# Kernel optimization log

Hardware: AMD Instinct MI355X
Metric: run time of the kernel (lower is better)

The kernel has to match this reference:

```python
import jax, jax.numpy as jnp
import numpy as np

N = 50000      # nodes
E = 800000     # edges (before self loops)
F_IN = 50      # PPI num_features
H = 4          # heads
C = 64         # hidden per head
NC = 121       # PPI num_classes
NEG_SLOPE = 0.2


def setup_inputs() -> dict:
    key = jax.random.key(0)
    ks = jax.random.split(key, 20)
    p = lambda k, shape: (jax.random.normal(k, shape, jnp.float32) * 0.1)
    x0 = jax.random.normal(ks[0], (N, F_IN), jnp.float32)
    edge_index = jax.random.randint(ks[1], (2, E), 0, N, dtype=jnp.int64)
    return dict(
        x0=x0, edge_index=edge_index,
        W1=p(ks[2], (F_IN, H * C)), as1=p(ks[3], (H, C)), ad1=p(ks[4], (H, C)),
        res1=p(ks[5], (F_IN, H * C)), b1=jnp.zeros((H * C,), jnp.float32),
        W2=p(ks[6], (H * C, H * C)), as2=p(ks[7], (H, C)), ad2=p(ks[8], (H, C)),
        res2=p(ks[9], (H * C, H * C)), b2=jnp.zeros((H * C,), jnp.float32),
        W3=p(ks[10], (H * C, H * NC)), as3=p(ks[11], (H, NC)), ad3=p(ks[12], (H, NC)),
        res3=p(ks[13], (H * C, NC)), b3=jnp.zeros((NC,), jnp.float32),
    )


def _gat(x, src, dst, W, a_src, a_dst, resW, b, concat):
    """PyG-style GATConv with residual, self loops already in (src, dst)."""
    n = x.shape[0]
    heads, outc = a_src.shape
    h = (x @ W).reshape(n, heads, outc)                 # [N,H,C]
    al_s = (h * a_src).sum(-1)                          # [N,H]
    al_d = (h * a_dst).sum(-1)                          # [N,H]
    e = jax.nn.leaky_relu(al_s[src] + al_d[dst], NEG_SLOPE)  # [E,H]
    m = jax.ops.segment_max(e, dst, num_segments=n)     # stable softmax per dst
    ex = jnp.exp(e - m[dst])
    denom = jax.ops.segment_sum(ex, dst, num_segments=n)
    alpha = ex / denom[dst]                             # [E,H]
    out = jax.ops.segment_sum(h[src] * alpha[:, :, None], dst, num_segments=n)  # [N,H,C]
    out = out.reshape(n, heads * outc) if concat else out.mean(axis=1)
    return out + x @ resW + b


def reference(x0, edge_index,
              W1, as1, ad1, res1, b1,
              W2, as2, ad2, res2, b2,
              W3, as3, ad3, res3, b3):
    n = x0.shape[0]
    loop = jnp.arange(n, dtype=edge_index.dtype)        # add self loops (PyG default)
    src = jnp.concatenate([edge_index[0], loop])
    dst = jnp.concatenate([edge_index[1], loop])
    x1 = jax.nn.relu(_gat(x0, src, dst, W1, as1, ad1, res1, b1, True))
    x2 = jax.nn.relu(_gat(x1, src, dst, W2, as2, ad2, res2, b2, True))
    x3 = _gat(x2, src, dst, W3, as3, ad3, res3, b3, False)
    return x3
```

## Files before the change

kernel.cpp:

```cpp
#include <hip/hip_runtime.h>

#define NNODES 50000
#define NEDGES 800000
#define NTOT   (NEDGES + NNODES)
#define F_IN   50
#define KPAD1  64
#define HEADS  4
#define C1     64
#define HC1    256
#define NC     121
#define K1S    320
#define K3S    1280
#define N2S    512
#define N2X    520
#define SLOTS  128

typedef unsigned short ushort_t;
typedef __attribute__((ext_vector_type(4))) unsigned short ushort4_t;
typedef __attribute__((ext_vector_type(8))) unsigned short ushort8;
typedef __attribute__((ext_vector_type(8))) __bf16 bf16x8;
typedef __attribute__((ext_vector_type(4))) float f32x4;
typedef __attribute__((ext_vector_type(4))) int int4_t;

__device__ __forceinline__ ushort_t f2bf(float f) {
    union { float f; unsigned int u; } v; v.f = f;
    unsigned int u = v.u;
    return (ushort_t)((u + 0x7fffu + ((u >> 16) & 1u)) >> 16);
}
__device__ __forceinline__ float bf2f(ushort_t s) {
    union { unsigned int u; float f; } v; v.u = ((unsigned int)s) << 16;
    return v.f;
}
__device__ __forceinline__ float lrelu(float x) { return x > 0.f ? x : 0.2f * x; }
__device__ __forceinline__ f32x4 cvt4lo(ushort8 v) {
    f32x4 r; r[0] = bf2f(v[0]); r[1] = bf2f(v[1]); r[2] = bf2f(v[2]); r[3] = bf2f(v[3]);
    return r;
}
__device__ __forceinline__ f32x4 cvt4hi(ushort8 v) {
    f32x4 r; r[0] = bf2f(v[4]); r[1] = bf2f(v[5]); r[2] = bf2f(v[6]); r[3] = bf2f(v[7]);
    return r;
}
__device__ __forceinline__ void wave_lds_sync() {
    asm volatile("s_waitcnt lgkmcnt(0)" ::: "memory");
}

__device__ __forceinline__ void scatter_body(int i, const int* __restrict__ ei,
                                             int* __restrict__ cnt,
                                             int* __restrict__ csr_src) {
    if (i >= NTOT) return;
    int s, d;
    if (i < NEDGES) { s = ei[i]; d = ei[NEDGES + i]; }
    else            { s = d = i - NEDGES; }
    if ((unsigned)d >= NNODES) d = 0;
    if ((unsigned)s >= NNODES) s = 0;
    int k = atomicAdd(&cnt[d], 1);
    if (k < SLOTS) csr_src[d * SLOTS + k] = s;
}

#define SZ_A (NNODES * KPAD1)
#define SZ_B (HC1 * K1S)
#define SZ_C (N2X * HC1)
#define SZ_D (N2X)
#define SZ_E (NC * K3S)
#define SZ_F (KPAD1 * 4)
#define SZ_G (HC1 * 4)
#define PREP_TOTAL (SZ_A + SZ_B + SZ_C + SZ_D + SZ_E + 2 * SZ_F + 2 * SZ_G)
#define PREP_BLK ((PREP_TOTAL + 255) / 256)
#define CNT_BLK  ((NTOT + 255) / 256)

__device__ void prep_body(int i,
                 const float* __restrict__ x0,
                 const float* __restrict__ W1, const float* __restrict__ res1,
                 const float* __restrict__ W2, const float* __restrict__ res2,
                 const float* __restrict__ W3, const float* __restrict__ res3,
                 const float* __restrict__ as1, const float* __restrict__ ad1,
                 const float* __restrict__ as2, const float* __restrict__ ad2,
                 const float* __restrict__ as3, const float* __restrict__ ad3,
                 const float* __restrict__ b2,
                 ushort_t* __restrict__ x0b, ushort_t* __restrict__ Bt1,
                 ushort_t* __restrict__ Bt2, ushort_t* __restrict__ Bt3,
                 float* __restrict__ bias520,
                 float* __restrict__ w_as1, float* __restrict__ w_ad1,
                 float* __restrict__ w_as3, float* __restrict__ w_ad3) {
    if (i < SZ_A) {
        int m = i >> 6, k = i & 63;
        x0b[i] = (k < F_IN) ? f2bf(x0[(size_t)m * F_IN + k]) : (ushort_t)0;
        return;
    }
    i -= SZ_A;
    if (i < SZ_B) {
        int c = i / K1S, kk = i - c * K1S;
        float v = 0.f;
        if (kk < 256) {
            int h = kk >> 6, k = kk & 63;
            if (k < F_IN && (c >> 6) == h) v = W1[(size_t)k * HC1 + c];
        } else {
            int k = kk - 256;
            if (k < F_IN) v = res1[(size_t)k * HC1 + c];
        }
        Bt1[i] = f2bf(v);
        return;
    }
    i -= SZ_B;
    if (i < SZ_C) {
        int c = i / HC1, k = i - c * HC1;
        float v;
        if (c < HC1) {
            v = W2[(size_t)k * HC1 + c];
        } else if (c < 512) {
            v = res2[(size_t)k * HC1 + (c - HC1)];
        } else {
            int j = c - 512;
            int h = j & 3;
            const float* a = (j < 4) ? as2 : ad2;
            float s = 0.f;
            for (int cc = 0; cc < C1; ++cc)
                s += W2[(size_t)k * HC1 + h * C1 + cc] * a[h * C1 + cc];
            v = s;
        }
        Bt2[i] = f2bf(v);
        return;
    }
    i -= SZ_C;
    if (i < SZ_D) {
        bias520[i] = (i >= HC1 && i < 512) ? b2[i - HC1] : 0.f;
        return;
    }
    i -= SZ_D;
    if (i < SZ_E) {
        int c = i / K3S, kk = i - c * K3S;
        float v;
        if (kk < 1024) {
            int h = kk >> 8, k = kk & 255;
            v = 0.25f * W3[(size_t)k * (HEADS * NC) + h * NC + c];
        } else {
            int k = kk - 1024;
            v = res3[(size_t)k * NC + c];
        }
        Bt3[i] = f2bf(v);
        return;
    }
    i -= SZ_E;
    if (i < 2 * SZ_F) {
        const float* a = (i < SZ_F) ? as1 : ad1;
        float* w = (i < SZ_F) ? w_as1 : w_ad1;
        int ii = (i < SZ_F) ? i : i - SZ_F;
        int k = ii >> 2, h = ii & 3;
        float s = 0.f;
        if (k < F_IN)
            for (int c = 0; c < C1; ++c) s += W1[(size_t)k * HC1 + h * C1 + c] * a[h * C1 + c];
        w[ii] = s;
        return;
    }
    i -= 2 * SZ_F;
    {
        int grp = i / SZ_G, ii = i - grp * SZ_G;
        int k = ii >> 2, h = ii & 3;
        const float* a = grp ? ad3 : as3;
        float s = 0.f;
        for (int c = 0; c < NC; ++c)
            s += W3[(size_t)k * (HEADS * NC) + h * NC + c] * a[h * NC + c];
        (grp ? w_ad3 : w_as3)[ii] = s;
    }
}

__global__ __launch_bounds__(256)
void prep_scatter_kernel(const float* __restrict__ x0,
                 const float* __restrict__ W1, const float* __restrict__ res1,
                 const float* __restrict__ W2, const float* __restrict__ res2,
                 const float* __restrict__ W3, const float* __restrict__ res3,
                 const float* __restrict__ as1, const float* __restrict__ ad1,
                 const float* __restrict__ as2, const float* __restrict__ ad2,
                 const float* __restrict__ as3, const float* __restrict__ ad3,
                 const float* __restrict__ b2,
                 ushort_t* __restrict__ x0b, ushort_t* __restrict__ Bt1,
                 ushort_t* __restrict__ Bt2, ushort_t* __restrict__ Bt3,
                 float* __restrict__ bias520,
                 float* __restrict__ w_as1, float* __restrict__ w_ad1,
                 float* __restrict__ w_as3, float* __restrict__ w_ad3,
                 const int* __restrict__ ei, int* __restrict__ cnt,
                 int* __restrict__ csr_src) {
    int b = blockIdx.x;
    if (b < PREP_BLK) {
        prep_body(b * 256 + threadIdx.x, x0, W1, res1, W2, res2, W3, res3,
                  as1, ad1, as2, ad2, as3, ad3, b2, x0b, Bt1, Bt2, Bt3,
                  bias520, w_as1, w_ad1, w_as3, w_ad3);
    } else {
        scatter_body((b - PREP_BLK) * 256 + threadIdx.x, ei, cnt, csr_src);
    }
}

#define BK 64
#define LDP (BK + 8)

__global__ __launch_bounds__(256)
void gemm64_kernel(const ushort_t* __restrict__ A1, int lda1,
                   const ushort_t* __restrict__ A2, int lda2, int Ksplit,
                   const ushort_t* __restrict__ Bt, const float* __restrict__ bias,
                   ushort_t* __restrict__ Cb,
                   int M, int N, int K, int relu) {
    __shared__ ushort_t As[64 * LDP];
    __shared__ ushort_t Bs[128 * LDP];
    int tid = threadIdx.x, lane = tid & 63, wid = tid >> 6;
    int l15 = lane & 15, q8 = (lane >> 4) * 8;
    int m0 = blockIdx.y * 64, n0 = blockIdx.x * 128;
    f32x4 c4[8] = {};
    for (int k0 = 0; k0 < K; k0 += BK) {
        #pragma unroll
        for (int it = 0; it < 2; ++it) {
            int c = tid + it * 256;
            int row = c >> 3, c8 = c & 7;
            int k = k0 + c8 * 8;
            ushort8 va = (ushort8)0;
            int gm = m0 + row;
            if (gm < M) {
                if (k < Ksplit) va = *(const ushort8*)&A1[(size_t)gm * lda1 + k];
                else            va = *(const ushort8*)&A2[(size_t)gm * lda2 + (k - Ksplit)];
            }
            *(ushort8*)&As[row * LDP + c8 * 8] = va;
        }
        #pragma unroll
        for (int it = 0; it < 4; ++it) {
            int c = tid + it * 256;
            int row = c >> 3, c8 = c & 7;
            int k = k0 + c8 * 8;
            ushort8 vb = (ushort8)0;
            int gn = n0 + row;
            if (gn < N) vb = *(const ushort8*)&Bt[(size_t)gn * K + k];
            *(ushort8*)&Bs[row * LDP + c8 * 8] = vb;
        }
        __syncthreads();
        #pragma unroll
        for (int kk = 0; kk < BK; kk += 32) {
            bf16x8 af = *(const bf16x8*)&As[(wid * 16 + l15) * LDP + kk + q8];
            #pragma unroll
            for (int ni = 0; ni < 8; ++ni) {
                bf16x8 bf = *(const bf16x8*)&Bs[(ni * 16 + l15) * LDP + kk + q8];
                c4[ni] = __builtin_amdgcn_mfma_f32_16x16x32_bf16(af, bf, c4[ni], 0, 0, 0);
            }
        }
        __syncthreads();
    }
    int rbase = m0 + wid * 16 + (lane >> 4) * 4;
    #pragma unroll
    for (int ni = 0; ni < 8; ++ni) {
        int col = n0 + ni * 16 + l15;
        if (col >= N) continue;
        float bv = bias ? bias[col] : 0.f;
        #pragma unroll
        for (int r = 0; r < 4; ++r) {
            int m = rbase + r;
            if (m >= M) continue;
            float v = c4[ni][r] + bv;
            if (relu) v = fmaxf(v, 0.f);
            Cb[(size_t)m * N + col] = f2bf(v);
        }
    }
}

__global__ __launch_bounds__(256)
void gemm2x64_kernel(const ushort_t* __restrict__ A,
                     const ushort_t* __restrict__ Bt,
                     const float* __restrict__ bias,
                     ushort_t* __restrict__ comb,
                     float* __restrict__ als, float* __restrict__ ald,
                     int M) {
    __shared__ ushort_t As[64 * LDP];
    __shared__ ushort_t Bs[128 * LDP];
    int tid = threadIdx.x, lane = tid & 63, wid = tid >> 6;
    int l15 = lane & 15, q8 = (lane >> 4) * 8;
    int m0 = blockIdx.y * 64, n0 = blockIdx.x * 128;
    f32x4 c4[8] = {};
    for (int k0 = 0; k0 < HC1; k0 += BK) {
        #pragma unroll
        for (int it = 0; it < 2; ++it) {
            int c = tid + it * 256;
            int row = c >> 3, c8 = c & 7;
            int k = k0 + c8 * 8;
            ushort8 va = (ushort8)0;
            int gm = m0 + row;
            if (gm < M) va = *(const ushort8*)&A[(size_t)gm * HC1 + k];
            *(ushort8*)&As[row * LDP + c8 * 8] = va;
        }
        #pragma unroll
        for (int it = 0; it < 4; ++it) {
            int c = tid + it * 256;
            int row = c >> 3, c8 = c & 7;
            int k = k0 + c8 * 8;
            ushort8 vb = (ushort8)0;
            int gn = n0 + row;
            if (gn < N2X) vb = *(const ushort8*)&Bt[(size_t)gn * HC1 + k];
            *(ushort8*)&Bs[row * LDP + c8 * 8] = vb;
        }
        __syncthreads();
        #pragma unroll
        for (int kk = 0; kk < BK; kk += 32) {
            bf16x8 af = *(const bf16x8*)&As[(wid * 16 + l15) * LDP + kk + q8];
            #pragma unroll
            for (int ni = 0; ni < 8; ++ni) {
                bf16x8 bf = *(const bf16x8*)&Bs[(ni * 16 + l15) * LDP + kk + q8];
                c4[ni] = __builtin_amdgcn_mfma_f32_16x16x32_bf16(af, bf, c4[ni], 0, 0, 0);
            }
        }
        __syncthreads();
    }
    int rbase = m0 + wid * 16 + (lane >> 4) * 4;
    #pragma unroll
    for (int ni = 0; ni < 8; ++ni) {
        int ncol = n0 + ni * 16 + l15;
        if (ncol >= N2X) continue;
        float bv = bias[ncol];
        #pragma unroll
        for (int r = 0; r < 4; ++r) {
            int m = rbase + r;
            if (m >= M) continue;
            float v = c4[ni][r] + bv;
            if (ncol < 512) {
                comb[(size_t)m * N2S + ncol] = f2bf(v);
            } else {
                int j = ncol - 512;
                if (j < 4) als[m * 4 + j] = v;
                else       ald[m * 4 + (j - 4)] = v;
            }
        }
    }
}

__global__ __launch_bounds__(256)
void gemm3s_kernel(const ushort_t* __restrict__ A1, int lda1,
                   const ushort_t* __restrict__ A2, int lda2, int Ksplit,
                   const ushort_t* __restrict__ Bt, const float* __restrict__ bias,
                   float* __restrict__ out, int M, int N, int K) {
    __shared__ ushort_t As[64 * LDP];
    __shared__ ushort_t Bs[128 * LDP];
    int tid = threadIdx.x, lane = tid & 63, wid = tid >> 6;
    int l15 = lane & 15, q8 = (lane >> 4) * 8;
    int m0 = blockIdx.x * 64;
    f32x4 c4[8] = {};
    for (int k0 = 0; k0 < K; k0 += BK) {
        #pragma unroll
        for (int it = 0; it < 2; ++it) {
            int c = tid + it * 256;
            int row = c >> 3, c8 = c & 7;
            int k = k0 + c8 * 8;
            ushort8 va = (ushort8)0;
            int gm = m0 + row;
            if (gm < M) {
                if (k < Ksplit) va = *(const ushort8*)&A1[(size_t)gm * lda1 + k];
                else            va = *(const ushort8*)&A2[(size_t)gm * lda2 + (k - Ksplit)];
            }
            *(ushort8*)&As[row * LDP + c8 * 8] = va;
        }
        #pragma unroll
        for (int it = 0; it < 4; ++it) {
            int c = tid + it * 256;
            int row = c >> 3, c8 = c & 7;
            int k = k0 + c8 * 8;
            ushort8 vb = (ushort8)0;
            if (row < N) vb = *(const ushort8*)&Bt[(size_t)row * K + k];
            *(ushort8*)&Bs[row * LDP + c8 * 8] = vb;
        }
        __syncthreads();
        #pragma unroll
        for (int kk = 0; kk < BK; kk += 32) {
            bf16x8 af = *(const bf16x8*)&As[(wid * 16 + l15) * LDP + kk + q8];
            #pragma unroll
            for (int ni = 0; ni < 8; ++ni) {
                bf16x8 bf = *(const bf16x8*)&Bs[(ni * 16 + l15) * LDP + kk + q8];
                c4[ni] = __builtin_amdgcn_mfma_f32_16x16x32_bf16(af, bf, c4[ni], 0, 0, 0);
            }
        }
        __syncthreads();
    }
    int rbase = m0 + wid * 16 + (lane >> 4) * 4;
    #pragma unroll
    for (int ni = 0; ni < 8; ++ni) {
        int col = ni * 16 + l15;
        if (col >= NC) continue;
        float bv = bias[col];
        #pragma unroll
        for (int r = 0; r < 4; ++r) {
            int m = rbase + r;
            if (m < M) out[(size_t)m * NC + col] = c4[ni][r] + bv;
        }
    }
}

__global__ __launch_bounds__(256)
void logits_gemv_kernel(const ushort_t* __restrict__ X, int K,
                        const float* __restrict__ w_as, const float* __restrict__ w_ad,
                        float* __restrict__ als, float* __restrict__ ald) {
    int wid = threadIdx.x >> 6, lane = threadIdx.x & 63;
    int n = blockIdx.x * 4 + wid;
    float ps[HEADS] = {}, pd[HEADS] = {};
    for (int k0 = lane * 4; k0 < K; k0 += 256) {
        ushort4_t xv = *(const ushort4_t*)&X[(size_t)n * K + k0];
        float x[4] = {bf2f(xv.x), bf2f(xv.y), bf2f(xv.z), bf2f(xv.w)};
        #pragma unroll
        for (int j = 0; j < 4; ++j) {
            #pragma unroll
            for (int h = 0; h < HEADS; ++h) {
                ps[h] += x[j] * w_as[(k0 + j) * 4 + h];
                pd[h] += x[j] * w_ad[(k0 + j) * 4 + h];
            }
        }
    }
    #pragma unroll
    for (int off = 32; off; off >>= 1)
        #pragma unroll
        for (int h = 0; h < HEADS; ++h) {
            ps[h] += __shfl_xor(ps[h], off);
            pd[h] += __shfl_xor(pd[h], off);
        }
    if (lane == 0)
        #pragma unroll
        for (int h = 0; h < HEADS; ++h) {
            als[n * HEADS + h] = ps[h];
            ald[n * HEADS + h] = pd[h];
        }
}

#define E_CHUNK32(ROWBYTES)                                                   \
    int i = base + l;                                                         \
    int nv = end - base; if (nv > 32) nv = 32;                                \
    if (i < end) {                                                            \
        int s = csr_src[i];                                                   \
        soffw[l] = s * (ROWBYTES);                                            \
        f32x4 av = *(const f32x4*)&als[s * 4];                                \
        f32x4 e;                                                              \
        _Pragma("unroll")                                                     \
        for (int h = 0; h < HEADS; ++h) {                                     \
            e[h] = __expf(lrelu(av[h] + aldd[h]));                            \
            den4[h] += e[h];                                                  \
        }                                                                     \
        *(f32x4*)&sew[l * 4] = e;                                             \
    }                                                                         \
    wave_lds_sync();

#define DEN_REDUCE16                                                          \
    _Pragma("unroll")                                                         \
    for (int off = 16; off; off >>= 1)                                        \
        _Pragma("unroll")                                                     \
        for (int h = 0; h < HEADS; ++h)                                       \
            den4[h] += __shfl_xor(den4[h], off);

__global__ __launch_bounds__(256)
void agg1_kernel(const ushort_t* __restrict__ x0b,
                 const float* __restrict__ als, const float* __restrict__ ald,
                 const int* __restrict__ cnt, const int* __restrict__ csr_src,
                 ushort_t* __restrict__ aggx) {
    __shared__ int   soff[8][32];
    __shared__ float se[8][32 * 4];
    int tid = threadIdx.x;
    int hw = tid >> 5, l = tid & 31;
    int d = blockIdx.x * 8 + hw;
    int* soffw = soff[hw];
    float* sew = se[hw];
    int beg = d * SLOTS;
    int deg = cnt[d]; if (deg > SLOTS) deg = SLOTS;
    int end = beg + deg;
    f32x4 aldd = *(const f32x4*)&ald[d * 4];
    f32x4 den4 = (f32x4)0.f;
    f32x4 acc0 = (f32x4)0.f, acc1 = (f32x4)0.f;
    int lb = l * 4;
    for (int base = beg; base < end; base += 32) {
        E_CHUNK32(KPAD1 * 2)
        int j = 0;
        for (; j + 4 <= nv; j += 4) {
            int4_t o = *(const int4_t*)&soffw[j];
            f32x4 e0 = *(const f32x4*)&sew[j * 4];
            f32x4 e1 = *(const f32x4*)&sew[(j + 1) * 4];
            f32x4 e2 = *(const f32x4*)&sew[(j + 2) * 4];
            f32x4 e3 = *(const f32x4*)&sew[(j + 3) * 4];
            unsigned int v0 = *(const unsigned int*)((const char*)x0b + o.x + lb);
            unsigned int v1 = *(const unsigned int*)((const char*)x0b + o.y + lb);
            unsigned int v2 = *(const unsigned int*)((const char*)x0b + o.z + lb);
            unsigned int v3 = *(const unsigned int*)((const char*)x0b + o.w + lb);
            acc0 += e0 * bf2f((ushort_t)(v0 & 0xffffu)) + e1 * bf2f((ushort_t)(v1 & 0xffffu))
                  + e2 * bf2f((ushort_t)(v2 & 0xffffu)) + e3 * bf2f((ushort_t)(v3 & 0xffffu));
            acc1 += e0 * bf2f((ushort_t)(v0 >> 16)) + e1 * bf2f((ushort_t)(v1 >> 16))
                  + e2 * bf2f((ushort_t)(v2 >> 16)) + e3 * bf2f((ushort_t)(v3 >> 16));
        }
        for (; j < nv; ++j) {
            int o = soffw[j];
            f32x4 e = *(const f32x4*)&sew[j * 4];
            unsigned int v = *(const unsigned int*)((const char*)x0b + o + lb);
            acc0 += e * bf2f((ushort_t)(v & 0xffffu));
            acc1 += e * bf2f((ushort_t)(v >> 16));
        }
        wave_lds_sync();
    }
    DEN_REDUCE16
    #pragma unroll
    for (int h = 0; h < HEADS; ++h) {
        float r = 1.f / den4[h];
        unsigned int pk = (unsigned int)f2bf(acc0[h] * r)
                        | ((unsigned int)f2bf(acc1[h] * r) << 16);
        *(unsigned int*)&aggx[(size_t)d * HC1 + h * 64 + l * 2] = pk;
    }
}

__global__ __launch_bounds__(256)
void agg2_kernel(const ushort_t* __restrict__ comb,
                 const float* __restrict__ als, const float* __restrict__ ald,
                 const int* __restrict__ cnt, const int* __restrict__ csr_src,
                 const float* __restrict__ w_as3, const float* __restrict__ w_ad3,
                 ushort_t* __restrict__ xnext,
                 float* __restrict__ als3, float* __restrict__ ald3) {
    __shared__ int   soff[8][32];
    __shared__ float se[8][32 * 4];
    int tid = threadIdx.x;
    int hw = tid >> 5, l = tid & 31;
    int d = blockIdx.x * 8 + hw;
    int* soffw = soff[hw];
    float* sew = se[hw];
    int hh = l >> 3;
    int beg = d * SLOTS;
    int deg = cnt[d]; if (deg > SLOTS) deg = SLOTS;
    int end = beg + deg;
    f32x4 aldd = *(const f32x4*)&ald[d * 4];
    f32x4 den4 = (f32x4)0.f;
    f32x4 acc[2] = {};
    int lb = l * 16;
    for (int base = beg; base < end; base += 32) {
        E_CHUNK32(N2S * 2)
        int j = 0;
        for (; j + 4 <= nv; j += 4) {
            int4_t o = *(const int4_t*)&soffw[j];
            ushort8 v0 = *(const ushort8*)((const char*)comb + o.x + lb);
            ushort8 v1 = *(const ushort8*)((const char*)comb + o.y + lb);
            ushort8 v2 = *(const ushort8*)((const char*)comb + o.z + lb);
            ushort8 v3 = *(const ushort8*)((const char*)comb + o.w + lb);
            float e0 = sew[j * 4 + hh], e1 = sew[(j + 1) * 4 + hh];
            float e2 = sew[(j + 2) * 4 + hh], e3 = sew[(j + 3) * 4 + hh];
            acc[0] += e0 * cvt4lo(v0) + e1 * cvt4lo(v1) + e2 * cvt4lo(v2) + e3 * cvt4lo(v3);
            acc[1] += e0 * cvt4hi(v0) + e1 * cvt4hi(v1) + e2 * cvt4hi(v2) + e3 * cvt4hi(v3);
        }
        for (; j < nv; ++j) {
            int o = soffw[j];
            float e = sew[j * 4 + hh];
            ushort8 v = *(const ushort8*)((const char*)comb + o + lb);
            acc[0] += e * cvt4lo(v);
            acc[1] += e * cvt4hi(v);
        }
        wave_lds_sync();
    }
    DEN_REDUCE16
    float r = 1.f / den4[hh];
    ushort8 rv = *(const ushort8*)&comb[(size_t)d * N2S + 256 + l * 8];
    float vout[8];
    ushort8 o8;
    #pragma unroll
    for (int q = 0; q < 2; ++q)
        #pragma unroll
        for (int c = 0; c < 4; ++c) {
            float vv = fmaxf(acc[q][c] * r + bf2f(rv[q * 4 + c]), 0.f);
            vout[q * 4 + c] = vv;
            o8[q * 4 + c] = f2bf(vv);
        }
    *(ushort8*)&xnext[(size_t)d * HC1 + l * 8] = o8;
    f32x4 ps = (f32x4)0.f, pd = (f32x4)0.f;
    #pragma unroll
    for (int cc = 0; cc < 8; ++cc) {
        int col = l * 8 + cc;
        f32x4 wsj = *(const f32x4*)&w_as3[col * 4];
        f32x4 wdj = *(const f32x4*)&w_ad3[col * 4];
        ps += vout[cc] * wsj;
        pd += vout[cc] * wdj;
    }
    #pragma unroll
    for (int off = 16; off; off >>= 1) {
        #pragma unroll
        for (int h = 0; h < HEADS; ++h) {
            ps[h] += __shfl_xor(ps[h], off);
            pd[h] += __shfl_xor(pd[h], off);
        }
    }
    if (l == 0) {
        *(f32x4*)&als3[d * 4] = ps;
        *(f32x4*)&ald3[d * 4] = pd;
    }
}

__global__ __launch_bounds__(256)
void agg3_kernel(const ushort_t* __restrict__ x2b,
                 const float* __restrict__ als, const float* __restrict__ ald,
                 const int* __restrict__ cnt, const int* __restrict__ csr_src,
                 ushort_t* __restrict__ aggx) {
    __shared__ int   soff[8][32];
    __shared__ float se[8][32 * 4];
    int tid = threadIdx.x;
    int hw = tid >> 5, l = tid & 31;
    int d = blockIdx.x * 8 + hw;
    int* soffw = soff[hw];
    float* sew = se[hw];
    int beg = d * SLOTS;
    int deg = cnt[d]; if (deg > SLOTS) deg = SLOTS;
    int end = beg + deg;
    f32x4 aldd = *(const f32x4*)&ald[d * 4];
    f32x4 den4 = (f32x4)0.f;
    f32x4 acc[HEADS][2] = {};
    int lb = l * 16;
    for (int base = beg; base < end; base += 32) {
        E_CHUNK32(HC1 * 2)
        int j = 0;
        for (; j + 4 <= nv; j += 4) {
            int4_t o = *(const int4_t*)&soffw[j];
            ushort8 v0 = *(const ushort8*)((const char*)x2b + o.x + lb);
            ushort8 v1 = *(const ushort8*)((const char*)x2b + o.y + lb);
            ushort8 v2 = *(const ushort8*)((const char*)x2b + o.z + lb);
            ushort8 v3 = *(const ushort8*)((const char*)x2b + o.w + lb);
            f32x4 e0 = *(const f32x4*)&sew[j * 4];
            f32x4 e1 = *(const f32x4*)&sew[(j + 1) * 4];
            f32x4 e2 = *(const f32x4*)&sew[(j + 2) * 4];
            f32x4 e3 = *(const f32x4*)&sew[(j + 3) * 4];
            f32x4 xl, xh;
            xl = cvt4lo(v0); xh = cvt4hi(v0);
            #pragma unroll
            for (int h = 0; h < HEADS; ++h) { acc[h][0] += e0[h] * xl; acc[h][1] += e0[h] * xh; }
            xl = cvt4lo(v1); xh = cvt4hi(v1);
            #pragma unroll
            for (int h = 0; h < HEADS; ++h) { acc[h][0] += e1[h] * xl; acc[h][1] += e1[h] * xh; }
            xl = cvt4lo(v2); xh = cvt4hi(v2);
            #pragma unroll
            for (int h = 0; h < HEADS; ++h) { acc[h][0] += e2[h] * xl; acc[h][1] += e2[h] * xh; }
            xl = cvt4lo(v3); xh = cvt4hi(v3);
            #pragma unroll
            for (int h = 0; h < HEADS; ++h) { acc[h][0] += e3[h] * xl; acc[h][1] += e3[h] * xh; }
        }
        for (; j < nv; ++j) {
            int o = soffw[j];
            f32x4 e = *(const f32x4*)&sew[j * 4];
            ushort8 v = *(const ushort8*)((const char*)x2b + o + lb);
            f32x4 xl = cvt4lo(v), xh = cvt4hi(v);
            #pragma unroll
            for (int h = 0; h < HEADS; ++h) { acc[h][0] += e[h] * xl; acc[h][1] += e[h] * xh; }
        }
        wave_lds_sync();
    }
    DEN_REDUCE16
    #pragma unroll
    for (int h = 0; h < HEADS; ++h) {
        float rdv = 1.f / den4[h];
        ushort8 ow;
        #pragma unroll
        for (int q = 0; q < 2; ++q)
            #pragma unroll
            for (int c = 0; c < 4; ++c)
                ow[q * 4 + c] = f2bf(acc[h][q][c] * rdv);
        *(ushort8*)&aggx[(size_t)d * 1024 + h * HC1 + l * 8] = ow;
    }
}

extern "C" void kernel_launch(void* const* d_in, const int* in_sizes, int n_in,
                              void* d_out, int out_size, void* d_ws, size_t ws_size,
                              hipStream_t stream) {
    const float* x0   = (const float*)d_in[0];
    const int*   ei   = (const int*)d_in[1];
    const float* W1   = (const float*)d_in[2];
    const float* as1  = (const float*)d_in[3];
    const float* ad1  = (const float*)d_in[4];
    const float* res1 = (const float*)d_in[5];
    const float* b1   = (const float*)d_in[6];
    const float* W2   = (const float*)d_in[7];
    const float* as2  = (const float*)d_in[8];
    const float* ad2  = (const float*)d_in[9];
    const float* res2 = (const float*)d_in[10];
    const float* b2   = (const float*)d_in[11];
    const float* W3   = (const float*)d_in[12];
    const float* as3  = (const float*)d_in[13];
    const float* ad3  = (const float*)d_in[14];
    const float* res3 = (const float*)d_in[15];
    const float* b3   = (const float*)d_in[16];

    char* p = (char*)d_ws;
    auto alloc = [&](size_t bytes) -> void* {
        void* r = (void*)p;
        p += (bytes + 255) & ~(size_t)255;
        return r;
    };
    int*      cnt     = (int*)alloc((size_t)NNODES * 4);
    int*      csr_src = (int*)alloc((size_t)NNODES * SLOTS * 4);
    float*    als     = (float*)alloc((size_t)NNODES * HEADS * 4);
    float*    ald     = (float*)alloc((size_t)NNODES * HEADS * 4);
    float*    als3    = (float*)alloc((size_t)NNODES * HEADS * 4);
    float*    ald3    = (float*)alloc((size_t)NNODES * HEADS * 4);
    ushort_t* x0b     = (ushort_t*)alloc((size_t)NNODES * KPAD1 * 2);
    ushort_t* x2      = (ushort_t*)alloc((size_t)NNODES * HC1 * 2);
    ushort_t* Bt1     = (ushort_t*)alloc((size_t)HC1 * K1S * 2);
    ushort_t* Bt2     = (ushort_t*)alloc((size_t)N2X * HC1 * 2);
    float*    bias520 = (float*)alloc((size_t)N2X * 4);
    ushort_t* Bt3     = (ushort_t*)alloc((size_t)NC * K3S * 2);
    float*    w_as1   = (float*)alloc((size_t)KPAD1 * 4 * 4);
    float*    w_ad1   = (float*)alloc((size_t)KPAD1 * 4 * 4);
    float*    w_as3   = (float*)alloc((size_t)HC1 * 4 * 4);
    float*    w_ad3   = (float*)alloc((size_t)HC1 * 4 * 4);
    char*     big     = (char*)alloc((size_t)NNODES * 1024 * 2);
    ushort_t* aggx1   = (ushort_t*)big;
    ushort_t* x1      = (ushort_t*)(big + (size_t)NNODES * HC1 * 2);
    ushort_t* comb    = (ushort_t*)(big + (size_t)NNODES * HC1 * 4);
    ushort_t* aggx3   = (ushort_t*)big;

    hipMemsetAsync(cnt, 0, (size_t)NNODES * 4, stream);

    prep_scatter_kernel<<<PREP_BLK + CNT_BLK, 256, 0, stream>>>(
        x0, W1, res1, W2, res2, W3, res3, as1, ad1, as2, ad2, as3, ad3, b2,
        x0b, Bt1, Bt2, Bt3, bias520, w_as1, w_ad1, w_as3, w_ad3,
        ei, cnt, csr_src);

    int nagg4 = NNODES / 4;
    int nagg8 = NNODES / 8;
    int mblk  = (NNODES + 63) / 64;

    logits_gemv_kernel<<<nagg4, 256, 0, stream>>>(x0b, KPAD1, w_as1, w_ad1, als, ald);
    agg1_kernel<<<nagg8, 256, 0, stream>>>(x0b, als, ald, cnt, csr_src, aggx1);
    {
        dim3 g(HC1 / 128, mblk);
        gemm64_kernel<<<g, 256, 0, stream>>>(aggx1, HC1, x0b, KPAD1, HC1,
                                             Bt1, b1, x1, NNODES, HC1, K1S, 1);
    }

    {
        dim3 g((N2X + 127) / 128, mblk);
        gemm2x64_kernel<<<g, 256, 0, stream>>>(x1, Bt2, bias520, comb, als, ald, NNODES);
    }
    agg2_kernel<<<nagg8, 256, 0, stream>>>(comb, als, ald, cnt, csr_src,
                                           w_as3, w_ad3, x2, als3, ald3);

    agg3_kernel<<<nagg8, 256, 0, stream>>>(x2, als3, ald3, cnt, csr_src, aggx3);
    gemm3s_kernel<<<mblk, 256, 0, stream>>>(
        aggx3, 1024, x2, HC1, 1024, Bt3, b3, (float*)d_out, NNODES, 128, K3S);
}
```

Baseline: 537.3 us.

## Fuse layer-1 attention logits into prep kernel and pad edge counters

Removes the separate layer-1 logits GEMV launch. The attention-folded weights are now computed per block in LDS and the logits are produced directly from fp32 x0 inside the combined prep/scatter kernel. The per-node degree counters are padded to 16-int stride to reduce atomic contention and false sharing, and scatter blocks are ordered first in the grid. In exchange, every gemv block recomputes the 400 small weight dot products, the cnt buffer and its memset grow 16x, and later kernels read counters strided.

```diff
diff --git a/kernel.cpp b/kernel.cpp
--- a/kernel.cpp
+++ b/kernel.cpp
@@ -14,6 +14,7 @@
 #define N2S    512
 #define N2X    520
 #define SLOTS  128
+#define CPAD   16
 
 typedef unsigned short ushort_t;
 typedef __attribute__((ext_vector_type(4))) unsigned short ushort4_t;
@@ -53,7 +54,7 @@
     else            { s = d = i - NEDGES; }
     if ((unsigned)d >= NNODES) d = 0;
     if ((unsigned)s >= NNODES) s = 0;
-    int k = atomicAdd(&cnt[d], 1);
+    int k = atomicAdd(&cnt[d * CPAD], 1);
     if (k < SLOTS) csr_src[d * SLOTS + k] = s;
 }
 
@@ -62,25 +63,23 @@
 #define SZ_C (N2X * HC1)
 #define SZ_D (N2X)
 #define SZ_E (NC * K3S)
-#define SZ_F (KPAD1 * 4)
 #define SZ_G (HC1 * 4)
-#define PREP_TOTAL (SZ_A + SZ_B + SZ_C + SZ_D + SZ_E + 2 * SZ_F + 2 * SZ_G)
+#define PREP_TOTAL (SZ_A + SZ_B + SZ_C + SZ_D + SZ_E + 2 * SZ_G)
 #define PREP_BLK ((PREP_TOTAL + 255) / 256)
-#define CNT_BLK  ((NTOT + 255) / 256)
+#define SCAT_BLK ((NTOT + 255) / 256)
+#define GEMV1_BLK ((NNODES + 63) / 64)
 
 __device__ void prep_body(int i,
                  const float* __restrict__ x0,
                  const float* __restrict__ W1, const float* __restrict__ res1,
                  const float* __restrict__ W2, const float* __restrict__ res2,
                  const float* __restrict__ W3, const float* __restrict__ res3,
-                 const float* __restrict__ as1, const float* __restrict__ ad1,
                  const float* __restrict__ as2, const float* __restrict__ ad2,
                  const float* __restrict__ as3, const float* __restrict__ ad3,
                  const float* __restrict__ b2,
                  ushort_t* __restrict__ x0b, ushort_t* __restrict__ Bt1,
                  ushort_t* __restrict__ Bt2, ushort_t* __restrict__ Bt3,
                  float* __restrict__ bias520,
-                 float* __restrict__ w_as1, float* __restrict__ w_ad1,
                  float* __restrict__ w_as3, float* __restrict__ w_ad3) {
     if (i < SZ_A) {
         int m = i >> 6, k = i & 63;
@@ -141,18 +140,6 @@
         return;
     }
     i -= SZ_E;
-    if (i < 2 * SZ_F) {
-        const float* a = (i < SZ_F) ? as1 : ad1;
-        float* w = (i < SZ_F) ? w_as1 : w_ad1;
-        int ii = (i < SZ_F) ? i : i - SZ_F;
-        int k = ii >> 2, h = ii & 3;
-        float s = 0.f;
-        if (k < F_IN)
-            for (int c = 0; c < C1; ++c) s += W1[(size_t)k * HC1 + h * C1 + c] * a[h * C1 + c];
-        w[ii] = s;
-        return;
-    }
-    i -= 2 * SZ_F;
     {
         int grp = i / SZ_G, ii = i - grp * SZ_G;
         int k = ii >> 2, h = ii & 3;
@@ -164,8 +151,49 @@
     }
 }
 
+__device__ void gemv1_body64(int b, int tid,
+                             const float* __restrict__ x0,
+                             const float* __restrict__ W1,
+                             const float* __restrict__ as1, const float* __restrict__ ad1,
+                             float* __restrict__ als, float* __restrict__ ald,
+                             float* lds_w ) {
+    if (tid >= 144) lds_w[tid + 256] = 0.f;
+    for (int idx = tid; idx < 400; idx += 256) {
+        int grp = idx >= 200 ? 1 : 0;
+        int ii = idx - grp * 200;
+        int k = ii >> 2, h = ii & 3;
+        const float* a = grp ? ad1 : as1;
+        float s = 0.f;
+        for (int c = 0; c < C1; ++c)
+            s += W1[(size_t)k * HC1 + h * C1 + c] * a[h * C1 + c];
+        lds_w[k * 8 + grp * 4 + h] = s;
+    }
+    __syncthreads();
+    int wid = tid >> 6, lane = tid & 63;
+    f32x4 was = *(const f32x4*)&lds_w[lane * 8];
+    f32x4 wad = *(const f32x4*)&lds_w[lane * 8 + 4];
+    #pragma unroll 4
+    for (int t = 0; t < 16; ++t) {
+        int n = b * 64 + wid * 16 + t;
+        if (n >= NNODES) break;
+        float xv = (lane < F_IN) ? x0[(size_t)n * F_IN + lane] : 0.f;
+        f32x4 ps = xv * was, pd = xv * wad;
+        #pragma unroll
+        for (int off = 32; off; off >>= 1)
+            #pragma unroll
+            for (int h = 0; h < HEADS; ++h) {
+                ps[h] += __shfl_xor(ps[h], off);
+                pd[h] += __shfl_xor(pd[h], off);
+            }
+        if (lane == 0) {
+            *(f32x4*)&als[n * 4] = ps;
+            *(f32x4*)&ald[n * 4] = pd;
+        }
+    }
+}
+
 __global__ __launch_bounds__(256)
-void prep_scatter_kernel(const float* __restrict__ x0,
+void prep_scatter_gemv_kernel(const float* __restrict__ x0,
                  const float* __restrict__ W1, const float* __restrict__ res1,
                  const float* __restrict__ W2, const float* __restrict__ res2,
                  const float* __restrict__ W3, const float* __restrict__ res3,
@@ -176,17 +204,21 @@
                  ushort_t* __restrict__ x0b, ushort_t* __restrict__ Bt1,
                  ushort_t* __restrict__ Bt2, ushort_t* __restrict__ Bt3,
                  float* __restrict__ bias520,
-                 float* __restrict__ w_as1, float* __restrict__ w_ad1,
                  float* __restrict__ w_as3, float* __restrict__ w_ad3,
                  const int* __restrict__ ei, int* __restrict__ cnt,
-                 int* __restrict__ csr_src) {
+                 int* __restrict__ csr_src,
+                 float* __restrict__ als, float* __restrict__ ald) {
+    __shared__ float lds_w[512];
     int b = blockIdx.x;
-    if (b < PREP_BLK) {
-        prep_body(b * 256 + threadIdx.x, x0, W1, res1, W2, res2, W3, res3,
-                  as1, ad1, as2, ad2, as3, ad3, b2, x0b, Bt1, Bt2, Bt3,
-                  bias520, w_as1, w_ad1, w_as3, w_ad3);
+    if (b < SCAT_BLK) {
+        scatter_body(b * 256 + threadIdx.x, ei, cnt, csr_src);
+    } else if (b < SCAT_BLK + PREP_BLK) {
+        prep_body((b - SCAT_BLK) * 256 + threadIdx.x, x0, W1, res1, W2, res2,
+                  W3, res3, as2, ad2, as3, ad3, b2, x0b, Bt1, Bt2, Bt3,
+                  bias520, w_as3, w_ad3);
     } else {
-        scatter_body((b - PREP_BLK) * 256 + threadIdx.x, ei, cnt, csr_src);
+        gemv1_body64(b - SCAT_BLK - PREP_BLK, threadIdx.x, x0, W1, as1, ad1,
+                     als, ald, lds_w);
     }
 }
 
@@ -384,40 +416,6 @@
             if (m < M) out[(size_t)m * NC + col] = c4[ni][r] + bv;
         }
     }
-}
-
-__global__ __launch_bounds__(256)
-void logits_gemv_kernel(const ushort_t* __restrict__ X, int K,
-                        const float* __restrict__ w_as, const float* __restrict__ w_ad,
-                        float* __restrict__ als, float* __restrict__ ald) {
-    int wid = threadIdx.x >> 6, lane = threadIdx.x & 63;
-    int n = blockIdx.x * 4 + wid;
-    float ps[HEADS] = {}, pd[HEADS] = {};
-    for (int k0 = lane * 4; k0 < K; k0 += 256) {
-        ushort4_t xv = *(const ushort4_t*)&X[(size_t)n * K + k0];
-        float x[4] = {bf2f(xv.x), bf2f(xv.y), bf2f(xv.z), bf2f(xv.w)};
-        #pragma unroll
-        for (int j = 0; j < 4; ++j) {
-            #pragma unroll
-            for (int h = 0; h < HEADS; ++h) {
-                ps[h] += x[j] * w_as[(k0 + j) * 4 + h];
-                pd[h] += x[j] * w_ad[(k0 + j) * 4 + h];
-            }
-        }
-    }
-    #pragma unroll
-    for (int off = 32; off; off >>= 1)
-        #pragma unroll
-        for (int h = 0; h < HEADS; ++h) {
-            ps[h] += __shfl_xor(ps[h], off);
-            pd[h] += __shfl_xor(pd[h], off);
-        }
-    if (lane == 0)
-        #pragma unroll
-        for (int h = 0; h < HEADS; ++h) {
-            als[n * HEADS + h] = ps[h];
-            ald[n * HEADS + h] = pd[h];
-        }
 }
 
 #define E_CHUNK32(ROWBYTES)                                                   \
@@ -457,7 +455,7 @@
     int* soffw = soff[hw];
     float* sew = se[hw];
     int beg = d * SLOTS;
-    int deg = cnt[d]; if (deg > SLOTS) deg = SLOTS;
+    int deg = cnt[d * CPAD]; if (deg > SLOTS) deg = SLOTS;
     int end = beg + deg;
     f32x4 aldd = *(const f32x4*)&ald[d * 4];
     f32x4 den4 = (f32x4)0.f;
@@ -516,7 +514,7 @@
     float* sew = se[hw];
     int hh = l >> 3;
     int beg = d * SLOTS;
-    int deg = cnt[d]; if (deg > SLOTS) deg = SLOTS;
+    int deg = cnt[d * CPAD]; if (deg > SLOTS) deg = SLOTS;
     int end = beg + deg;
     f32x4 aldd = *(const f32x4*)&ald[d * 4];
     f32x4 den4 = (f32x4)0.f;
@@ -595,7 +593,7 @@
     int* soffw = soff[hw];
     float* sew = se[hw];
     int beg = d * SLOTS;
-    int deg = cnt[d]; if (deg > SLOTS) deg = SLOTS;
+    int deg = cnt[d * CPAD]; if (deg > SLOTS) deg = SLOTS;
     int end = beg + deg;
     f32x4 aldd = *(const f32x4*)&ald[d * 4];
     f32x4 den4 = (f32x4)0.f;
@@ -679,7 +677,7 @@
         p += (bytes + 255) & ~(size_t)255;
         return r;
     };
-    int*      cnt     = (int*)alloc((size_t)NNODES * 4);
+    int*      cnt     = (int*)alloc((size_t)NNODES * CPAD * 4);
     int*      csr_src = (int*)alloc((size_t)NNODES * SLOTS * 4);
     float*    als     = (float*)alloc((size_t)NNODES * HEADS * 4);
     float*    ald     = (float*)alloc((size_t)NNODES * HEADS * 4);
@@ -691,8 +689,6 @@
     ushort_t* Bt2     = (ushort_t*)alloc((size_t)N2X * HC1 * 2);
     float*    bias520 = (float*)alloc((size_t)N2X * 4);
     ushort_t* Bt3     = (ushort_t*)alloc((size_t)NC * K3S * 2);
-    float*    w_as1   = (float*)alloc((size_t)KPAD1 * 4 * 4);
-    float*    w_ad1   = (float*)alloc((size_t)KPAD1 * 4 * 4);
     float*    w_as3   = (float*)alloc((size_t)HC1 * 4 * 4);
     float*    w_ad3   = (float*)alloc((size_t)HC1 * 4 * 4);
     char*     big     = (char*)alloc((size_t)NNODES * 1024 * 2);
@@ -701,18 +697,16 @@
     ushort_t* comb    = (ushort_t*)(big + (size_t)NNODES * HC1 * 4);
     ushort_t* aggx3   = (ushort_t*)big;
 
-    hipMemsetAsync(cnt, 0, (size_t)NNODES * 4, stream);
-
-    prep_scatter_kernel<<<PREP_BLK + CNT_BLK, 256, 0, stream>>>(
+    hipMemsetAsync(cnt, 0, (size_t)NNODES * CPAD * 4, stream);
+
+    prep_scatter_gemv_kernel<<<SCAT_BLK + PREP_BLK + GEMV1_BLK, 256, 0, stream>>>(
         x0, W1, res1, W2, res2, W3, res3, as1, ad1, as2, ad2, as3, ad3, b2,
-        x0b, Bt1, Bt2, Bt3, bias520, w_as1, w_ad1, w_as3, w_ad3,
-        ei, cnt, csr_src);
-
-    int nagg4 = NNODES / 4;
+        x0b, Bt1, Bt2, Bt3, bias520, w_as3, w_ad3,
+        ei, cnt, csr_src, als, ald);
+
     int nagg8 = NNODES / 8;
     int mblk  = (NNODES + 63) / 64;
 
-    logits_gemv_kernel<<<nagg4, 256, 0, stream>>>(x0b, KPAD1, w_as1, w_ad1, als, ald);
     agg1_kernel<<<nagg8, 256, 0, stream>>>(x0b, als, ald, cnt, csr_src, aggx1);
     {
         dim3 g(HC1 / 128, mblk);
```

Measured after the change: 594.7 us. +10.7%, slower.
